# Optimization experiments

Hardware: AMD Instinct MI355X
Metric: run time of the kernel (lower is better)

Reference implementation:

```python
import jax, jax.numpy as jnp
import numpy as np


def setup_inputs() -> dict:
    key = jax.random.key(0)
    k1, k2 = jax.random.split(key)
    N, M, D = 16384, 16384, 3
    src_V = jax.random.normal(k1, (N, D), dtype=jnp.float32)
    tar_V = jax.random.normal(k2, (M, D), dtype=jnp.float32)
    return {"src_V": src_V, "tar_V": tar_V}


def reference(src_V, tar_V):
    # 1-NN: for each target point find nearest source point (replaces cKDTree).
    # Squared distances via ||t||^2 - 2 t.s + ||s||^2 ; [M, N]
    d2 = (
        jnp.sum(tar_V * tar_V, axis=1, keepdims=True)
        - 2.0 * (tar_V @ src_V.T)
        + jnp.sum(src_V * src_V, axis=1)[None, :]
    )
    ii = jnp.argmin(d2, axis=1)            # [M] nearest src index per target
    diff = src_V[ii] - tar_V               # [M, 3]
    loss = 0.5 * jnp.sum(diff * diff)
    return loss
```

## Files before the change

kernel.cpp:

```cpp
#include <hip/hip_runtime.h>
#include <math.h>

constexpr int N_SRC = 16384;
constexpr int M_TAR = 16384;

constexpr int BLOCKS = M_TAR / 32;
constexpr int TPB = 1024;
constexpr int CHUNKS = 256;
constexpr int TILE = 4096;
constexpr int TILES = N_SRC / TILE;
constexpr int IPT = TILE / CHUNKS / 2;

__global__ void zero_out(float* __restrict__ out) {
    if (threadIdx.x == 0) out[0] = 0.0f;
}

__device__ __forceinline__ float embed_ao(float t, unsigned mask_v, unsigned row_s) {
    float r;
    asm("v_and_or_b32 %0, %1, %2, %3"
        : "=v"(r) : "v"(t), "v"(mask_v), "s"(row_s));
    return r;
}
__device__ __forceinline__ void min3(float& b, float e0, float e1) {
    asm("v_min3_f32 %0, %1, %2, %3"
        : "=v"(b) : "v"(b), "v"(e0), "v"(e1));
}

__global__ __launch_bounds__(TPB, 8) void nn6(const float* __restrict__ src,
                                              const float* __restrict__ tar,
                                              float* __restrict__ out) {
    __shared__ float4 tile[TILE];

    const int tid   = threadIdx.x;
    const int g     = tid & 3;
    const int chunk = tid >> 2;
    const int tbase = blockIdx.x * 32;

    float txm2[8], tym2[8], tzm2[8], best[8];
#pragma unroll
    for (int k = 0; k < 8; ++k) {
        int T = tbase + g + 4 * k;
        txm2[k] = -2.0f * tar[3 * T + 0];
        tym2[k] = -2.0f * tar[3 * T + 1];
        tzm2[k] = -2.0f * tar[3 * T + 2];
        best[k] = INFINITY;
    }

    unsigned mask_v = 0xFFFFFFC0u;

    for (int tl = 0; tl < TILES; ++tl) {
#pragma unroll
        for (int r = 0; r < TILE / TPB; ++r) {
            int p  = tid + r * TPB;
            int j3 = 3 * (tl * TILE + p);
            float x = src[j3 + 0], y = src[j3 + 1], z = src[j3 + 2];
            tile[p] = make_float4(x, y, z, fmaf(x, x, fmaf(y, y, z * z)));
        }
        __syncthreads();

#pragma unroll
        for (int i = 0; i < IPT; ++i) {
            float4 s0 = tile[(2 * i + 0) * CHUNKS + chunk];
            float4 s1 = tile[(2 * i + 1) * CHUNKS + chunk];
            unsigned row0 = (unsigned)(tl * 2 * IPT + 2 * i + 0);
            unsigned row1 = (unsigned)(tl * 2 * IPT + 2 * i + 1);
#pragma unroll
            for (int k = 0; k < 8; ++k) {
                float t0 = fmaf(s0.z, tzm2[k], s0.w);
                t0 = fmaf(s0.y, tym2[k], t0);
                t0 = fmaf(s0.x, txm2[k], t0);
                float t1 = fmaf(s1.z, tzm2[k], s1.w);
                t1 = fmaf(s1.y, tym2[k], t1);
                t1 = fmaf(s1.x, txm2[k], t1);
                float e0 = embed_ao(t0, mask_v, row0);
                float e1 = embed_ao(t1, mask_v, row1);
                min3(best[k], e0, e1);
            }
        }
        __syncthreads();
    }

    float* fv = (float*)tile;
    int*   fj = (int*)tile + 32 * 256;
#pragma unroll
    for (int k = 0; k < 8; ++k) {
        unsigned b = __float_as_uint(best[k]);
        int j  = (int)((b & 63u) * CHUNKS + chunk);
        int lt = g + 4 * k;
        fv[lt * CHUNKS + chunk] = __uint_as_float(b & 0xFFFFFFC0u);
        fj[lt * CHUNKS + chunk] = j;
    }
    __syncthreads();

    const int tprime = tid >> 5;
    const int sub    = tid & 31;
    float bv = fv[tprime * CHUNKS + sub];
    int   bj = fj[tprime * CHUNKS + sub];
#pragma unroll
    for (int m = 1; m < 8; ++m) {
        float v = fv[tprime * CHUNKS + sub + 32 * m];
        int   j = fj[tprime * CHUNKS + sub + 32 * m];
        if (v < bv) { bv = v; bj = j; }
    }
#pragma unroll
    for (int s = 16; s >= 1; s >>= 1) {
        float vv = __shfl_xor(bv, s, 64);
        int   jj = __shfl_xor(bj, s, 64);
        if (vv < bv) { bv = vv; bj = jj; }
    }
    __syncthreads();

    if (sub == 0) {
        int tt = tbase + tprime;
        float dx = src[3 * bj + 0] - tar[3 * tt + 0];
        float dy = src[3 * bj + 1] - tar[3 * tt + 1];
        float dz = src[3 * bj + 2] - tar[3 * tt + 2];
        fv[tprime] = 0.5f * fmaf(dx, dx, fmaf(dy, dy, dz * dz));
    }
    __syncthreads();
    if (tid == 0) {
        float ssum = 0.0f;
#pragma unroll
        for (int i = 0; i < 32; ++i) ssum += fv[i];
        atomicAdd(out, ssum);
    }
}

extern "C" void kernel_launch(void* const* d_in, const int* in_sizes, int n_in,
                              void* d_out, int out_size, void* d_ws, size_t ws_size,
                              hipStream_t stream) {
    const float* src = (const float*)d_in[0];
    const float* tar = (const float*)d_in[1];
    float* out = (float*)d_out;
    (void)d_ws; (void)ws_size;

    zero_out<<<1, 64, 0, stream>>>(out);
    nn6<<<BLOCKS, TPB, 0, stream>>>(src, tar, out);
}
```

Baseline: 90.19 us.

## Replace brute-force NN scan with uniform-grid spatial search

Swaps the all-pairs distance scan for a two-kernel approach. A single-block kernel bins the source points into a 16^3 uniform grid via counting sort. A search kernel then expands shells around each target's cell, using 8 lanes per target, with box lower-bound pruning and early termination. This removes the O(N*M) work but adds a serial single-block build, divergent irregular loops, and reliance on the Gaussian data mostly falling inside [-4,4].

Result: slower. 157.2 us (+74.3%).

```diff
diff --git a/kernel.cpp b/kernel.cpp
--- a/kernel.cpp
+++ b/kernel.cpp
@@ -4,125 +4,162 @@
 constexpr int N_SRC = 16384;
 constexpr int M_TAR = 16384;
 
-constexpr int BLOCKS = M_TAR / 32;
-constexpr int TPB = 1024;
-constexpr int CHUNKS = 256;
-constexpr int TILE = 4096;
-constexpr int TILES = N_SRC / TILE;
-constexpr int IPT = TILE / CHUNKS / 2;
 
-__global__ void zero_out(float* __restrict__ out) {
-    if (threadIdx.x == 0) out[0] = 0.0f;
+constexpr int   G     = 16;
+constexpr int   NCELL = G * G * G;
+constexpr float GLO   = -4.0f;
+constexpr float H     = 0.5f;
+constexpr float INVH  = 2.0f;
+
+constexpr int BUILD_TPB = 1024;
+constexpr int PPT_B     = N_SRC / BUILD_TPB;
+
+constexpr int TPB2    = 256;
+constexpr int LANES   = 8;
+constexpr int TGTPB   = TPB2 / LANES;
+constexpr int BLOCKS2 = M_TAR / TGTPB;
+
+__device__ __forceinline__ int cell_of(float v) {
+    int c = (int)floorf((v - GLO) * INVH);
+    return min(max(c, 0), G - 1);
 }
 
-__device__ __forceinline__ float embed_ao(float t, unsigned mask_v, unsigned row_s) {
-    float r;
-    asm("v_and_or_b32 %0, %1, %2, %3"
-        : "=v"(r) : "v"(t), "v"(mask_v), "s"(row_s));
-    return r;
-}
-__device__ __forceinline__ void min3(float& b, float e0, float e1) {
-    asm("v_min3_f32 %0, %1, %2, %3"
-        : "=v"(b) : "v"(b), "v"(e0), "v"(e1));
-}
+__global__ __launch_bounds__(BUILD_TPB, 1)
+void build(const float* __restrict__ src,
+           int* __restrict__ cellStart,
+           float4* __restrict__ pts,
+           float* __restrict__ out) {
+    __shared__ int cnt[NCELL];
+    __shared__ int psum[BUILD_TPB];
+    __shared__ int start[NCELL + 1];
+    const int tid = threadIdx.x;
+    if (tid == 0) out[0] = 0.0f;
+#pragma unroll
+    for (int r = 0; r < NCELL / BUILD_TPB; ++r) cnt[tid + r * BUILD_TPB] = 0;
+    __syncthreads();
 
-__global__ __launch_bounds__(TPB, 8) void nn6(const float* __restrict__ src,
-                                              const float* __restrict__ tar,
-                                              float* __restrict__ out) {
-    __shared__ float4 tile[TILE];
-
-    const int tid   = threadIdx.x;
-    const int g     = tid & 3;
-    const int chunk = tid >> 2;
-    const int tbase = blockIdx.x * 32;
-
-    float txm2[8], tym2[8], tzm2[8], best[8];
+    int cids[PPT_B];
 #pragma unroll
-    for (int k = 0; k < 8; ++k) {
-        int T = tbase + g + 4 * k;
-        txm2[k] = -2.0f * tar[3 * T + 0];
-        tym2[k] = -2.0f * tar[3 * T + 1];
-        tzm2[k] = -2.0f * tar[3 * T + 2];
-        best[k] = INFINITY;
-    }
-
-    unsigned mask_v = 0xFFFFFFC0u;
-
-    for (int tl = 0; tl < TILES; ++tl) {
-#pragma unroll
-        for (int r = 0; r < TILE / TPB; ++r) {
-            int p  = tid + r * TPB;
-            int j3 = 3 * (tl * TILE + p);
-            float x = src[j3 + 0], y = src[j3 + 1], z = src[j3 + 2];
-            tile[p] = make_float4(x, y, z, fmaf(x, x, fmaf(y, y, z * z)));
-        }
-        __syncthreads();
-
-#pragma unroll
-        for (int i = 0; i < IPT; ++i) {
-            float4 s0 = tile[(2 * i + 0) * CHUNKS + chunk];
-            float4 s1 = tile[(2 * i + 1) * CHUNKS + chunk];
-            unsigned row0 = (unsigned)(tl * 2 * IPT + 2 * i + 0);
-            unsigned row1 = (unsigned)(tl * 2 * IPT + 2 * i + 1);
-#pragma unroll
-            for (int k = 0; k < 8; ++k) {
-                float t0 = fmaf(s0.z, tzm2[k], s0.w);
-                t0 = fmaf(s0.y, tym2[k], t0);
-                t0 = fmaf(s0.x, txm2[k], t0);
-                float t1 = fmaf(s1.z, tzm2[k], s1.w);
-                t1 = fmaf(s1.y, tym2[k], t1);
-                t1 = fmaf(s1.x, txm2[k], t1);
-                float e0 = embed_ao(t0, mask_v, row0);
-                float e1 = embed_ao(t1, mask_v, row1);
-                min3(best[k], e0, e1);
-            }
-        }
-        __syncthreads();
-    }
-
-    float* fv = (float*)tile;
-    int*   fj = (int*)tile + 32 * 256;
-#pragma unroll
-    for (int k = 0; k < 8; ++k) {
-        unsigned b = __float_as_uint(best[k]);
-        int j  = (int)((b & 63u) * CHUNKS + chunk);
-        int lt = g + 4 * k;
-        fv[lt * CHUNKS + chunk] = __uint_as_float(b & 0xFFFFFFC0u);
-        fj[lt * CHUNKS + chunk] = j;
+    for (int r = 0; r < PPT_B; ++r) {
+        int i = tid + r * BUILD_TPB;
+        const float* q = src + 3 * i;
+        int cid = (cell_of(q[2]) * G + cell_of(q[1])) * G + cell_of(q[0]);
+        cids[r] = cid;
+        atomicAdd(&cnt[cid], 1);
     }
     __syncthreads();
 
-    const int tprime = tid >> 5;
-    const int sub    = tid & 31;
-    float bv = fv[tprime * CHUNKS + sub];
-    int   bj = fj[tprime * CHUNKS + sub];
-#pragma unroll
-    for (int m = 1; m < 8; ++m) {
-        float v = fv[tprime * CHUNKS + sub + 32 * m];
-        int   j = fj[tprime * CHUNKS + sub + 32 * m];
-        if (v < bv) { bv = v; bj = j; }
+    psum[tid] = cnt[4 * tid] + cnt[4 * tid + 1] + cnt[4 * tid + 2] + cnt[4 * tid + 3];
+    __syncthreads();
+    for (int off = 1; off < BUILD_TPB; off <<= 1) {
+        int v = (tid >= off) ? psum[tid - off] : 0;
+        __syncthreads();
+        psum[tid] += v;
+        __syncthreads();
     }
-#pragma unroll
-    for (int s = 16; s >= 1; s >>= 1) {
-        float vv = __shfl_xor(bv, s, 64);
-        int   jj = __shfl_xor(bj, s, 64);
-        if (vv < bv) { bv = vv; bj = jj; }
-    }
+    int s0 = (tid == 0) ? 0 : psum[tid - 1];
+    int s1 = s0 + cnt[4 * tid + 0];
+    int s2 = s1 + cnt[4 * tid + 1];
+    int s3 = s2 + cnt[4 * tid + 2];
+    start[4 * tid + 0] = s0;
+    start[4 * tid + 1] = s1;
+    start[4 * tid + 2] = s2;
+    start[4 * tid + 3] = s3;
+    if (tid == 0) start[NCELL] = N_SRC;
+    __syncthreads();
+    for (int i = tid; i < NCELL + 1; i += BUILD_TPB) cellStart[i] = start[i];
     __syncthreads();
 
-    if (sub == 0) {
-        int tt = tbase + tprime;
-        float dx = src[3 * bj + 0] - tar[3 * tt + 0];
-        float dy = src[3 * bj + 1] - tar[3 * tt + 1];
-        float dz = src[3 * bj + 2] - tar[3 * tt + 2];
-        fv[tprime] = 0.5f * fmaf(dx, dx, fmaf(dy, dy, dz * dz));
+#pragma unroll
+    for (int r = 0; r < PPT_B; ++r) {
+        int i = tid + r * BUILD_TPB;
+        const float* q = src + 3 * i;
+        float x = q[0], y = q[1], z = q[2];
+        int pos = atomicAdd(&start[cids[r]], 1);
+        pts[pos] = make_float4(x, y, z, 0.0f);
     }
+}
+
+__global__ __launch_bounds__(TPB2, 4)
+void nn_grid(const int* __restrict__ cellStart,
+             const float4* __restrict__ pts,
+             const float* __restrict__ tar,
+             float* __restrict__ out) {
+    __shared__ int   cs[NCELL + 1];
+    __shared__ float term[TGTPB];
+    const int tid = threadIdx.x;
+    for (int i = tid; i < NCELL + 1; i += TPB2) cs[i] = cellStart[i];
+    __syncthreads();
+
+    const int sub = tid & (LANES - 1);
+    const int T   = blockIdx.x * TGTPB + (tid >> 3);
+    const float tx = tar[3 * T + 0], ty = tar[3 * T + 1], tz = tar[3 * T + 2];
+    const int cx = cell_of(tx), cy = cell_of(ty), cz = cell_of(tz);
+
+    float best = 1e30f;
+    for (int R = 0; R < G; ++R) {
+        const float bestR = best;
+        const float thr   = fmaf(bestR, 1.0001f, 1e-6f);
+        const int zlo = max(cz - R, 0), zhi = min(cz + R, G - 1);
+        const int ylo = max(cy - R, 0), yhi = min(cy + R, G - 1);
+        const int xlo = max(cx - R, 0), xhi = min(cx + R, G - 1);
+        for (int nz = zlo; nz <= zhi; ++nz) {
+            int az = nz - cz; az = az < 0 ? -az : az;
+            for (int ny = ylo; ny <= yhi; ++ny) {
+                int ay = ny - cy; ay = ay < 0 ? -ay : ay;
+                for (int nx = xlo; nx <= xhi; ++nx) {
+                    int ax = nx - cx; ax = ax < 0 ? -ax : ax;
+                    int ch = max(ax, max(ay, az));
+                    if (ch != R) continue;
+                    float lox = (nx == 0)     ? -1e30f : GLO + nx * H;
+                    float hix = (nx == G - 1) ?  1e30f : GLO + (nx + 1) * H;
+                    float loy = (ny == 0)     ? -1e30f : GLO + ny * H;
+                    float hiy = (ny == G - 1) ?  1e30f : GLO + (ny + 1) * H;
+                    float loz = (nz == 0)     ? -1e30f : GLO + nz * H;
+                    float hiz = (nz == G - 1) ?  1e30f : GLO + (nz + 1) * H;
+                    float ddx = tx - fminf(fmaxf(tx, lox), hix);
+                    float ddy = ty - fminf(fmaxf(ty, loy), hiy);
+                    float ddz = tz - fminf(fmaxf(tz, loz), hiz);
+                    float dlb = fmaf(ddx, ddx, fmaf(ddy, ddy, ddz * ddz));
+                    if (dlb > thr) continue;
+                    int cid = (nz * G + ny) * G + nx;
+                    int s = cs[cid], e = cs[cid + 1];
+                    int j = s + sub;
+                    if (j < e) {
+                        float4 p = pts[j];
+                        for (j += LANES; j < e; j += LANES) {
+                            float4 pn = pts[j];
+                            float dx = p.x - tx, dy = p.y - ty, dz = p.z - tz;
+                            best = fminf(best, fmaf(dx, dx, fmaf(dy, dy, dz * dz)));
+                            p = pn;
+                        }
+                        float dx = p.x - tx, dy = p.y - ty, dz = p.z - tz;
+                        best = fminf(best, fmaf(dx, dx, fmaf(dy, dy, dz * dz)));
+                    }
+                }
+            }
+        }
+        best = fminf(best, __shfl_xor(best, 1, 64));
+        best = fminf(best, __shfl_xor(best, 2, 64));
+        best = fminf(best, __shfl_xor(best, 4, 64));
+        float dmin = 1e30f;
+        if (cx - R > 0)     dmin = fminf(dmin, tx - (GLO + (cx - R) * H));
+        if (cx + R < G - 1) dmin = fminf(dmin, (GLO + (cx + R + 1) * H) - tx);
+        if (cy - R > 0)     dmin = fminf(dmin, ty - (GLO + (cy - R) * H));
+        if (cy + R < G - 1) dmin = fminf(dmin, (GLO + (cy + R + 1) * H) - ty);
+        if (cz - R > 0)     dmin = fminf(dmin, tz - (GLO + (cz - R) * H));
+        if (cz + R < G - 1) dmin = fminf(dmin, (GLO + (cz + R + 1) * H) - tz);
+        if (dmin > 9e29f) break;
+        if (dmin * dmin > fmaf(best, 1.0001f, 1e-6f)) break;
+    }
+
+    if (sub == 0) term[tid >> 3] = 0.5f * best;
     __syncthreads();
     if (tid == 0) {
-        float ssum = 0.0f;
+        float s = 0.0f;
 #pragma unroll
-        for (int i = 0; i < 32; ++i) ssum += fv[i];
-        atomicAdd(out, ssum);
+        for (int i = 0; i < TGTPB; ++i) s += term[i];
+        atomicAdd(out, s);
     }
 }
 
@@ -132,8 +169,10 @@
     const float* src = (const float*)d_in[0];
     const float* tar = (const float*)d_in[1];
     float* out = (float*)d_out;
-    (void)d_ws; (void)ws_size;
+    int*    cellStart = (int*)d_ws;
+    float4* pts = (float4*)((char*)d_ws + 65536);
+    (void)ws_size;
 
-    zero_out<<<1, 64, 0, stream>>>(out);
-    nn6<<<BLOCKS, TPB, 0, stream>>>(src, tar, out);
+    build<<<1, BUILD_TPB, 0, stream>>>(src, cellStart, pts, out);
+    nn_grid<<<BLOCKS2, TPB2, 0, stream>>>(cellStart, pts, tar, out);
 }
```
